# Kernel tuning notes

Measured on AMD Instinct MI355X. Metric: run time of the kernel, lower is better.

## Reference

```python
import jax, jax.numpy as jnp
import numpy as np

EPS = 1e-5

def _layernorm(x, gamma, beta):
    mu = jnp.mean(x, axis=-1, keepdims=True)
    var = jnp.var(x, axis=-1, keepdims=True)
    return (x - mu) * jax.lax.rsqrt(var + EPS) * gamma + beta

def setup_inputs() -> dict:
    key = jax.random.key(0)
    ks = jax.random.split(key, 8)
    B, I, H = 8192, 1024, 1024
    s_w = 1.0 / np.sqrt(I)
    s_u = 1.0 / np.sqrt(H)
    return {
        "x": jax.random.normal(ks[0], (B, I), jnp.float32),
        "h": jax.random.normal(ks[1], (B, H), jnp.float32),
        "c": jax.random.normal(ks[2], (B, H), jnp.float32),
        "W_w": jax.random.uniform(ks[3], (I, 4 * H), jnp.float32, -s_w, s_w),
        "W_b": jax.random.uniform(ks[4], (4 * H,), jnp.float32, -s_w, s_w),
        "U_w": jax.random.uniform(ks[5], (H, 4 * H), jnp.float32, -s_u, s_u),
        "ln_g_gamma": jnp.ones((4 * H,), jnp.float32),
        "ln_g_beta": jnp.zeros((4 * H,), jnp.float32),
        "ln_c_gamma": jnp.ones((H,), jnp.float32),
        "ln_c_beta": jnp.zeros((H,), jnp.float32),
    }

def reference(x, h, c, W_w, W_b, U_w, ln_g_gamma, ln_g_beta, ln_c_gamma, ln_c_beta):
    gates_x = x @ W_w + W_b            # [B, 4H]
    gates_h = h @ U_w                  # [B, 4H]
    gates = gates_x + gates_h + gates_x * gates_h  # multiplicative integration
    gates = _layernorm(gates, ln_g_gamma, ln_g_beta)
    i, f, g, o = jnp.split(gates, 4, axis=-1)
    i = jax.nn.sigmoid(i)
    f = jax.nn.sigmoid(f)
    o = jax.nn.sigmoid(o)
    g = jnp.tanh(g)
    c_new = f * c + i * g
    c_new = _layernorm(c_new, ln_c_gamma, ln_c_beta)
    h_new = o * jnp.tanh(c_new)
    return (h_new, h_new, c_new)
```

## Files before the change

### kernel.cpp

```cpp
#include <hip/hip_runtime.h>
#include <hip/hip_fp16.h>
#include <cstdint>


#define MB (1024ull * 1024ull)

typedef short bf16x8 __attribute__((ext_vector_type(8)));
typedef float f32x4  __attribute__((ext_vector_type(4)));

__device__ __forceinline__ bool bf16_mode(const void* g1) {
    return ((const unsigned short*)g1)[0] == 0x3F80u;
}
__device__ __forceinline__ float b2f(unsigned short u) {
    union { unsigned int i; float f; } v; v.i = ((unsigned int)u) << 16; return v.f;
}
__device__ __forceinline__ unsigned short f2b(float f) {
    unsigned int i = __float_as_uint(f);
    unsigned int r = (i + 0x7FFFu + ((i >> 16) & 1u)) >> 16;
    return (unsigned short)r;
}
__device__ __forceinline__ unsigned short f2h(float f) {
    __half h = __float2half_rn(f);
    return *(unsigned short*)&h;
}
__device__ __forceinline__ void uph8(uint4 v, float* o) {
    unsigned int w[4] = { v.x, v.y, v.z, v.w };
#pragma unroll
    for (int q = 0; q < 4; ++q) {
        __half2 h = *(__half2*)&w[q];
        float2 f = __half22float2(h);
        o[2 * q] = f.x; o[2 * q + 1] = f.y;
    }
}
__device__ __forceinline__ void up4(uint2 v, float* o) {
    o[0] = __uint_as_float(v.x << 16);
    o[1] = __uint_as_float(v.x & 0xFFFF0000u);
    o[2] = __uint_as_float(v.y << 16);
    o[3] = __uint_as_float(v.y & 0xFFFF0000u);
}
__device__ __forceinline__ unsigned int pack2(unsigned short a, unsigned short b) {
    return (unsigned int)a | ((unsigned int)b << 16);
}
__device__ __forceinline__ void ld4(const void* p, size_t idx, bool isbf, float* o) {
    if (isbf) up4(*(const uint2*)((const unsigned short*)p + idx), o);
    else { float4 v = *(const float4*)((const float*)p + idx); o[0]=v.x; o[1]=v.y; o[2]=v.z; o[3]=v.w; }
}
__device__ __forceinline__ float fast_sigmoid(float z) { return 1.f / (1.f + __expf(-z)); }
__device__ __forceinline__ float fast_tanh(float z)    { return 1.f - 2.f / (__expf(2.f * z) + 1.f); }

__device__ __forceinline__ void load_lds16(const unsigned short* g, unsigned short* l) {
    __builtin_amdgcn_global_load_lds(
        (const __attribute__((address_space(1))) unsigned int*)g,
        (__attribute__((address_space(3))) unsigned int*)l,
        16, 0, 0);
}

__global__ __launch_bounds__(256)
void prep_weights(const void* __restrict__ Ww, const void* __restrict__ Uw,
                  const void* __restrict__ g1,
                  unsigned short* __restrict__ Wt, unsigned short* __restrict__ Ut)
{
    const bool isbf = bf16_mode(g1);
    const void* src = blockIdx.z ? Uw : Ww;
    unsigned short* dst = blockIdx.z ? Ut : Wt;
    __shared__ unsigned short tile[64][68];
    const int t  = threadIdx.x;
    const int tx = t & 15;
    const int ty = t >> 4;
    const int bx = blockIdx.x * 64;
    const int by = blockIdx.y * 64;
    if (isbf) {
        const unsigned short* s = (const unsigned short*)src;
#pragma unroll
        for (int it = 0; it < 4; ++it) {
            const int r = ty + it * 16;
            uint2 v = *(const uint2*)(s + (size_t)(by + r) * 4096 + bx + tx * 4);
            tile[r][tx * 4 + 0] = (unsigned short)(v.x & 0xFFFFu);
            tile[r][tx * 4 + 1] = (unsigned short)(v.x >> 16);
            tile[r][tx * 4 + 2] = (unsigned short)(v.y & 0xFFFFu);
            tile[r][tx * 4 + 3] = (unsigned short)(v.y >> 16);
        }
    } else {
        const float* s = (const float*)src;
#pragma unroll
        for (int it = 0; it < 4; ++it) {
            const int r = ty + it * 16;
            float4 v = *(const float4*)(s + (size_t)(by + r) * 4096 + bx + tx * 4);
            tile[r][tx * 4 + 0] = f2b(v.x);
            tile[r][tx * 4 + 1] = f2b(v.y);
            tile[r][tx * 4 + 2] = f2b(v.z);
            tile[r][tx * 4 + 3] = f2b(v.w);
        }
    }
    __syncthreads();
#pragma unroll
    for (int it = 0; it < 4; ++it) {
        const int rn = ty + it * 16;
        const int ck = tx * 4;
        uint2 w;
        w.x = pack2(tile[ck + 0][rn], tile[ck + 1][rn]);
        w.y = pack2(tile[ck + 2][rn], tile[ck + 3][rn]);
        *(uint2*)(dst + (size_t)(bx + rn) * 1024 + by + ck) = w;
    }
}

__global__ __launch_bounds__(256)
void prep_xh(const void* __restrict__ X, const void* __restrict__ Hs,
             const void* __restrict__ g1, void* __restrict__ outb)
{
    if (bf16_mode(g1)) return;
    const float* src = (blockIdx.y == 0) ? (const float*)X : (const float*)Hs;
    unsigned short* dst = (unsigned short*)((char*)outb + (blockIdx.y == 0 ? 48 * MB : 80 * MB));
    const size_t i0 = ((size_t)blockIdx.x * 256 + threadIdx.x) * 8;
    float4 a = *(const float4*)(src + i0);
    float4 b = *(const float4*)(src + i0 + 4);
    uint4 o;
    o.x = pack2(f2b(a.x), f2b(a.y));
    o.y = pack2(f2b(a.z), f2b(a.w));
    o.z = pack2(f2b(b.x), f2b(b.y));
    o.w = pack2(f2b(b.z), f2b(b.w));
    *(uint4*)(dst + i0) = o;
}

__global__ __launch_bounds__(512, 2)
void milstm_gemm(const void* __restrict__ Xraw, const void* __restrict__ Hraw,
                 const void* __restrict__ g1, const void* __restrict__ outb,
                 const unsigned short* __restrict__ Wt,
                 const unsigned short* __restrict__ Ut,
                 unsigned short* __restrict__ Gx, unsigned short* __restrict__ Gh,
                 int m0)
{
    const bool isbf = bf16_mode(g1);
    const int  z    = blockIdx.z;
    const unsigned short* A = z
        ? (isbf ? (const unsigned short*)Hraw : (const unsigned short*)((const char*)outb + 80 * MB))
        : (isbf ? (const unsigned short*)Xraw : (const unsigned short*)((const char*)outb + 48 * MB));
    const unsigned short* Bm = z ? Ut : Wt;
    unsigned short* Gout = z ? Gh : Gx;

    __shared__ __align__(16) unsigned short lds[4][2][8192];

    const int t    = threadIdx.x;
    const int wave = t >> 6;
    const int lane = t & 63;
    const int quad = lane >> 4;
    const int l16  = lane & 15;
    const int wm2  = wave >> 2;
    const int wn4  = wave & 3;

    const int nwg  = gridDim.x * gridDim.y;
    const int wgid = blockIdx.y * gridDim.x + blockIdx.x;
    const int swz  = (wgid & 7) * (nwg >> 3) + (wgid >> 3);
    const int bm   = (swz >> 4) * 256;
    const int bn   = (swz & 15) * 256;

    const int kbsw = (((t & 3) ^ ((t >> 3) & 3)) * 8);
    const unsigned short* sa0 = A  + (size_t)(m0 + bm + (t >> 2)) * 1024 + kbsw;
    const unsigned short* sb0 = Bm + (size_t)(bn + (t >> 2)) * 1024 + kbsw;

#define STAGE(tile, buf) do {                                        \
        const int ko_ = (tile) * 32;                                 \
        load_lds16(sa0 + ko_,          &lds[buf][0][t * 8]);         \
        load_lds16(sa0 + 131072 + ko_, &lds[buf][0][4096 + t * 8]);  \
        load_lds16(sb0 + ko_,          &lds[buf][1][t * 8]);         \
        load_lds16(sb0 + 131072 + ko_, &lds[buf][1][4096 + t * 8]);  \
    } while (0)

    const int kread = (quad ^ ((l16 >> 1) & 3)) * 8;
    const int raoff = (wm2 * 128 + l16) * 32 + kread;
    const int rboff = (wn4 * 64 + l16) * 32 + kread;

#define LDA(DST, BUF) do { _Pragma("unroll")                                  \
        for (int mi = 0; mi < 8; ++mi)                                        \
            DST[mi] = *(const bf16x8*)(&lds[BUF][0][0] + raoff + mi * 512);   \
    } while (0)
#define LDB(DST, BUF) do { _Pragma("unroll")                                  \
        for (int ni = 0; ni < 4; ++ni)                                        \
            DST[ni] = *(const bf16x8*)(&lds[BUF][1][0] + rboff + ni * 512);   \
    } while (0)

#define BAR()  __builtin_amdgcn_s_barrier()
#define VM4()  asm volatile("s_waitcnt vmcnt(4)" ::: "memory")
#define MFMA32(AV, BV) do {                                                   \
        __builtin_amdgcn_s_setprio(1);                                        \
        _Pragma("unroll")                                                     \
        for (int mi = 0; mi < 8; ++mi)                                        \
            _Pragma("unroll")                                                 \
            for (int ni = 0; ni < 4; ++ni)                                    \
                acc[mi][ni] = __builtin_amdgcn_mfma_f32_16x16x32_bf16(        \
                    AV[mi], BV[ni], acc[mi][ni], 0, 0, 0);                    \
        __builtin_amdgcn_s_setprio(0);                                        \
    } while (0)

    f32x4 acc[8][4] = {};
    bf16x8 aP[8], bP[4], aQ[8], bQ[4];

    STAGE(0, 0);
    STAGE(1, 1);
    STAGE(2, 2);
    asm volatile("s_waitcnt vmcnt(8)" ::: "memory");
    BAR();
    LDA(aP, 0); LDB(bP, 0);

    for (int ii = 0; ii < 8; ++ii) {
        const int q = 4 * ii;
        VM4(); BAR();
        STAGE((q + 3) & 31, 3);
        LDA(aQ, 1); LDB(bQ, 1);
        MFMA32(aP, bP);
        VM4(); BAR();
        STAGE((q + 4) & 31, 0);
        LDA(aP, 2); LDB(bP, 2);
        MFMA32(aQ, bQ);
        VM4(); BAR();
        STAGE((q + 5) & 31, 1);
        LDA(aQ, 3); LDB(bQ, 3);
        MFMA32(aP, bP);
        VM4(); BAR();
        STAGE((q + 6) & 31, 2);
        LDA(aP, 0); LDB(bP, 0);
        MFMA32(aQ, bQ);
    }
#undef STAGE
#undef LDA
#undef LDB
#undef BAR
#undef VM4
#undef MFMA32

    const int col0 = bn + wn4 * 64 + l16;
#pragma unroll
    for (int mi = 0; mi < 8; ++mi) {
        const int row0 = bm + wm2 * 128 + mi * 16 + quad * 4;
#pragma unroll
        for (int ni = 0; ni < 4; ++ni) {
            const int col = col0 + ni * 16;
#pragma unroll
            for (int r = 0; r < 4; ++r)
                Gout[(size_t)(row0 + r) * 4096 + col] = f2h(acc[mi][ni][r]);
        }
    }
}

__global__ __launch_bounds__(256)
void milstm_cell(const unsigned short* __restrict__ Gx,
                 const unsigned short* __restrict__ Gh,
                 const void* __restrict__ Wbr,
                 const void* __restrict__ C,
                 const void* __restrict__ g1, const void* __restrict__ b1,
                 const void* __restrict__ g2, const void* __restrict__ b2,
                 void* __restrict__ outb, int m0)
{
    const bool isbf = bf16_mode(g1);
    const int lrow = blockIdx.x;
    const int row  = m0 + lrow;
    const int tid  = threadIdx.x;
    const int lane = tid & 63;
    const int wave = tid >> 6;
    const uint4* gx4 = (const uint4*)(Gx + (size_t)lrow * 4096);
    const uint4* gh4 = (const uint4*)(Gh + (size_t)lrow * 4096);

    __shared__ __align__(16) float srow[4096];
    __shared__ float red[16];

    float s = 0.f, ss = 0.f;
#pragma unroll
    for (int u = 0; u < 2; ++u) {
        const int gbase = (tid * 2 + u) * 8;
        float fx[8], fh[8], bb[8];
        uph8(gx4[tid * 2 + u], fx);
        uph8(gh4[tid * 2 + u], fh);
        ld4(Wbr, gbase, isbf, bb);
        ld4(Wbr, gbase + 4, isbf, bb + 4);
        float g[8];
#pragma unroll
        for (int k = 0; k < 8; ++k) {
            const float ax = fx[k] + bb[k];
            const float v  = ax + fh[k] + ax * fh[k];
            g[k] = v;
            s  += v;
            ss += v * v;
        }
        *(float4*)&srow[gbase]     = make_float4(g[0], g[1], g[2], g[3]);
        *(float4*)&srow[gbase + 4] = make_float4(g[4], g[5], g[6], g[7]);
    }
#pragma unroll
    for (int off = 32; off > 0; off >>= 1) {
        s  += __shfl_xor(s, off, 64);
        ss += __shfl_xor(ss, off, 64);
    }
    if (lane == 0) { red[wave] = s; red[8 + wave] = ss; }
    __syncthreads();
    s  = red[0] + red[1] + red[2] + red[3];
    ss = red[8] + red[9] + red[10] + red[11];
    const float mu   = s * (1.f / 4096.f);
    const float rstd = rsqrtf(fmaxf(ss * (1.f / 4096.f) - mu * mu, 0.f) + 1e-5f);

    const int j0 = tid * 4;
    float xi[4], xf[4], xg[4], cc[4];
    float G1[4], B1[4], ii[4], cn[4], ov[4];

    { float4 v = *(const float4*)&srow[j0];        xi[0]=v.x; xi[1]=v.y; xi[2]=v.z; xi[3]=v.w; }
    { float4 v = *(const float4*)&srow[1024 + j0]; xf[0]=v.x; xf[1]=v.y; xf[2]=v.z; xf[3]=v.w; }
    { float4 v = *(const float4*)&srow[2048 + j0]; xg[0]=v.x; xg[1]=v.y; xg[2]=v.z; xg[3]=v.w; }
    { float4 v = *(const float4*)&srow[3072 + j0]; ov[0]=v.x; ov[1]=v.y; ov[2]=v.z; ov[3]=v.w; }
    ld4(C, (size_t)row * 1024 + j0, isbf, cc);

    ld4(g1, j0, isbf, G1); ld4(b1, j0, isbf, B1);
#pragma unroll
    for (int q = 0; q < 4; ++q) ii[q] = fast_sigmoid((xi[q] - mu) * rstd * G1[q] + B1[q]);
    ld4(g1, 1024 + j0, isbf, G1); ld4(b1, 1024 + j0, isbf, B1);
#pragma unroll
    for (int q = 0; q < 4; ++q) xf[q] = fast_sigmoid((xf[q] - mu) * rstd * G1[q] + B1[q]);
    ld4(g1, 2048 + j0, isbf, G1); ld4(b1, 2048 + j0, isbf, B1);
#pragma unroll
    for (int q = 0; q < 4; ++q) xg[q] = fast_tanh((xg[q] - mu) * rstd * G1[q] + B1[q]);
    ld4(g1, 3072 + j0, isbf, G1); ld4(b1, 3072 + j0, isbf, B1);
#pragma unroll
    for (int q = 0; q < 4; ++q) ov[q] = fast_sigmoid((ov[q] - mu) * rstd * G1[q] + B1[q]);
#pragma unroll
    for (int q = 0; q < 4; ++q) cn[q] = xf[q] * cc[q] + ii[q] * xg[q];

    float s2  = cn[0] + cn[1] + cn[2] + cn[3];
    float ss2 = cn[0]*cn[0] + cn[1]*cn[1] + cn[2]*cn[2] + cn[3]*cn[3];
#pragma unroll
    for (int off = 32; off > 0; off >>= 1) {
        s2  += __shfl_xor(s2, off, 64);
        ss2 += __shfl_xor(ss2, off, 64);
    }
    if (lane == 0) { red[4 + wave] = s2; red[12 + wave] = ss2; }
    __syncthreads();
    s2  = red[4]  + red[5]  + red[6]  + red[7];
    ss2 = red[12] + red[13] + red[14] + red[15];
    const float mu2   = s2 * (1.f / 1024.f);
    const float rstd2 = rsqrtf(fmaxf(ss2 * (1.f / 1024.f) - mu2 * mu2, 0.f) + 1e-5f);

    ld4(g2, j0, isbf, G1);
    ld4(b2, j0, isbf, B1);

    float hv[4], cv[4];
#pragma unroll
    for (int q = 0; q < 4; ++q) {
        cv[q] = (cn[q] - mu2) * rstd2 * G1[q] + B1[q];
        hv[q] = ov[q] * fast_tanh(cv[q]);
    }

    const size_t BH = (size_t)8192 * 1024;
    if (isbf) {
        unsigned short* out = (unsigned short*)outb;
        uint2 hb, cb;
        hb.x = pack2(f2b(hv[0]), f2b(hv[1])); hb.y = pack2(f2b(hv[2]), f2b(hv[3]));
        cb.x = pack2(f2b(cv[0]), f2b(cv[1])); cb.y = pack2(f2b(cv[2]), f2b(cv[3]));
        *(uint2*)(out + (size_t)row * 1024 + j0)          = hb;
        *(uint2*)(out + BH + (size_t)row * 1024 + j0)     = hb;
        *(uint2*)(out + 2 * BH + (size_t)row * 1024 + j0) = cb;
    } else {
        float* out = (float*)outb;
        float4 hf = { hv[0], hv[1], hv[2], hv[3] };
        float4 cf = { cv[0], cv[1], cv[2], cv[3] };
        *(float4*)(out + (size_t)row * 1024 + j0)          = hf;
        *(float4*)(out + BH + (size_t)row * 1024 + j0)     = hf;
        *(float4*)(out + 2 * BH + (size_t)row * 1024 + j0) = cf;
    }
}

extern "C" void kernel_launch(void* const* d_in, const int* in_sizes, int n_in,
                              void* d_out, int out_size, void* d_ws, size_t ws_size,
                              hipStream_t stream)
{
    const void* X  = d_in[0];
    const void* Hh = d_in[1];
    const void* C  = d_in[2];
    const void* Ww = d_in[3];
    const void* Wb = d_in[4];
    const void* Uw = d_in[5];
    const void* g1 = d_in[6];
    const void* b1 = d_in[7];
    const void* g2 = d_in[8];
    const void* b2 = d_in[9];

    const int P  = (ws_size >= 144 * MB) ? 1 : ((ws_size >= 80 * MB) ? 2 : 4);
    const int MR = 8192 / P;
    const size_t gsz = (size_t)MR * 4096;
    unsigned short* Gx = (unsigned short*)d_ws;
    unsigned short* Gh = Gx + gsz;
    unsigned short* Wt = Gh + gsz;
    unsigned short* Ut = Wt + (size_t)4096 * 1024;

    prep_weights<<<dim3(64, 16, 2), 256, 0, stream>>>(Ww, Uw, g1, Wt, Ut);
    prep_xh<<<dim3(4096, 2), 256, 0, stream>>>(X, Hh, g1, d_out);

    for (int ph = 0; ph < P; ++ph) {
        const int m0 = ph * MR;
        milstm_gemm<<<dim3(16, MR / 256, 2), 512, 0, stream>>>(
            X, Hh, g1, d_out, Wt, Ut, Gx, Gh, m0);
        milstm_cell<<<dim3(MR), 256, 0, stream>>>(
            Gx, Gh, Wb, C, g1, b1, g2, b2, d_out, m0);
    }
}
```

Before: 417.7 us.

## Merge prep kernels, fold bias into GEMM epilogue, use one wave per row in cell

The two preprocessing kernels become one launch that dispatches on block index, removing a launch. The x-side bias is added in the GEMM epilogue before the fp16 store, so the cell kernel no longer loads W_b. The cell kernel now gives each row to a single wave that keeps all 4096 gate values in registers. This drops the LDS staging buffer and both block-level syncs, in exchange for higher register pressure per thread. Adding the bias before rounding to fp16 also changes numerics slightly.

```diff
diff --git a/kernel.cpp b/kernel.cpp
--- a/kernel.cpp
+++ b/kernel.cpp
@@ -32,18 +32,20 @@
         o[2 * q] = f.x; o[2 * q + 1] = f.y;
     }
 }
-__device__ __forceinline__ void up4(uint2 v, float* o) {
-    o[0] = __uint_as_float(v.x << 16);
-    o[1] = __uint_as_float(v.x & 0xFFFF0000u);
-    o[2] = __uint_as_float(v.y << 16);
-    o[3] = __uint_as_float(v.y & 0xFFFF0000u);
-}
 __device__ __forceinline__ unsigned int pack2(unsigned short a, unsigned short b) {
     return (unsigned int)a | ((unsigned int)b << 16);
 }
 __device__ __forceinline__ void ld4(const void* p, size_t idx, bool isbf, float* o) {
-    if (isbf) up4(*(const uint2*)((const unsigned short*)p + idx), o);
-    else { float4 v = *(const float4*)((const float*)p + idx); o[0]=v.x; o[1]=v.y; o[2]=v.z; o[3]=v.w; }
+    if (isbf) {
+        uint2 v = *(const uint2*)((const unsigned short*)p + idx);
+        o[0] = __uint_as_float(v.x << 16);
+        o[1] = __uint_as_float(v.x & 0xFFFF0000u);
+        o[2] = __uint_as_float(v.y << 16);
+        o[3] = __uint_as_float(v.y & 0xFFFF0000u);
+    } else {
+        float4 v = *(const float4*)((const float*)p + idx);
+        o[0]=v.x; o[1]=v.y; o[2]=v.z; o[3]=v.w;
+    }
 }
 __device__ __forceinline__ float fast_sigmoid(float z) { return 1.f / (1.f + __expf(-z)); }
 __device__ __forceinline__ float fast_tanh(float z)    { return 1.f - 2.f / (__expf(2.f * z) + 1.f); }
@@ -56,75 +58,82 @@
 }
 
 __global__ __launch_bounds__(256)
-void prep_weights(const void* __restrict__ Ww, const void* __restrict__ Uw,
-                  const void* __restrict__ g1,
-                  unsigned short* __restrict__ Wt, unsigned short* __restrict__ Ut)
+void milstm_prep(const void* __restrict__ Ww, const void* __restrict__ Uw,
+                 const void* __restrict__ X, const void* __restrict__ Hs,
+                 const void* __restrict__ g1,
+                 unsigned short* __restrict__ Wt, unsigned short* __restrict__ Ut,
+                 void* __restrict__ outb)
 {
     const bool isbf = bf16_mode(g1);
-    const void* src = blockIdx.z ? Uw : Ww;
-    unsigned short* dst = blockIdx.z ? Ut : Wt;
+    const int bid = blockIdx.x;
+    const int t   = threadIdx.x;
     __shared__ unsigned short tile[64][68];
-    const int t  = threadIdx.x;
-    const int tx = t & 15;
-    const int ty = t >> 4;
-    const int bx = blockIdx.x * 64;
-    const int by = blockIdx.y * 64;
-    if (isbf) {
-        const unsigned short* s = (const unsigned short*)src;
+
+    if (bid < 2048) {
+        const int wz  = bid >> 10;
+        const int idx = bid & 1023;
+        const int bx  = (idx & 63) * 64;
+        const int by  = (idx >> 6) * 64;
+        const void* src = wz ? Uw : Ww;
+        unsigned short* dst = wz ? Ut : Wt;
+        const int tx = t & 15;
+        const int ty = t >> 4;
+        if (isbf) {
+            const unsigned short* s = (const unsigned short*)src;
+#pragma unroll
+            for (int it = 0; it < 4; ++it) {
+                const int r = ty + it * 16;
+                uint2 v = *(const uint2*)(s + (size_t)(by + r) * 4096 + bx + tx * 4);
+                tile[r][tx * 4 + 0] = (unsigned short)(v.x & 0xFFFFu);
+                tile[r][tx * 4 + 1] = (unsigned short)(v.x >> 16);
+                tile[r][tx * 4 + 2] = (unsigned short)(v.y & 0xFFFFu);
+                tile[r][tx * 4 + 3] = (unsigned short)(v.y >> 16);
+            }
+        } else {
+            const float* s = (const float*)src;
+#pragma unroll
+            for (int it = 0; it < 4; ++it) {
+                const int r = ty + it * 16;
+                float4 v = *(const float4*)(s + (size_t)(by + r) * 4096 + bx + tx * 4);
+                tile[r][tx * 4 + 0] = f2b(v.x);
+                tile[r][tx * 4 + 1] = f2b(v.y);
+                tile[r][tx * 4 + 2] = f2b(v.z);
+                tile[r][tx * 4 + 3] = f2b(v.w);
+            }
+        }
+        __syncthreads();
 #pragma unroll
         for (int it = 0; it < 4; ++it) {
-            const int r = ty + it * 16;
-            uint2 v = *(const uint2*)(s + (size_t)(by + r) * 4096 + bx + tx * 4);
-            tile[r][tx * 4 + 0] = (unsigned short)(v.x & 0xFFFFu);
-            tile[r][tx * 4 + 1] = (unsigned short)(v.x >> 16);
-            tile[r][tx * 4 + 2] = (unsigned short)(v.y & 0xFFFFu);
-            tile[r][tx * 4 + 3] = (unsigned short)(v.y >> 16);
+            const int rn = ty + it * 16;
+            const int ck = tx * 4;
+            uint2 w;
+            w.x = pack2(tile[ck + 0][rn], tile[ck + 1][rn]);
+            w.y = pack2(tile[ck + 2][rn], tile[ck + 3][rn]);
+            *(uint2*)(dst + (size_t)(bx + rn) * 1024 + by + ck) = w;
         }
     } else {
-        const float* s = (const float*)src;
-#pragma unroll
-        for (int it = 0; it < 4; ++it) {
-            const int r = ty + it * 16;
-            float4 v = *(const float4*)(s + (size_t)(by + r) * 4096 + bx + tx * 4);
-            tile[r][tx * 4 + 0] = f2b(v.x);
-            tile[r][tx * 4 + 1] = f2b(v.y);
-            tile[r][tx * 4 + 2] = f2b(v.z);
-            tile[r][tx * 4 + 3] = f2b(v.w);
-        }
-    }
-    __syncthreads();
-#pragma unroll
-    for (int it = 0; it < 4; ++it) {
-        const int rn = ty + it * 16;
-        const int ck = tx * 4;
-        uint2 w;
-        w.x = pack2(tile[ck + 0][rn], tile[ck + 1][rn]);
-        w.y = pack2(tile[ck + 2][rn], tile[ck + 3][rn]);
-        *(uint2*)(dst + (size_t)(bx + rn) * 1024 + by + ck) = w;
-    }
-}
-
-__global__ __launch_bounds__(256)
-void prep_xh(const void* __restrict__ X, const void* __restrict__ Hs,
-             const void* __restrict__ g1, void* __restrict__ outb)
-{
-    if (bf16_mode(g1)) return;
-    const float* src = (blockIdx.y == 0) ? (const float*)X : (const float*)Hs;
-    unsigned short* dst = (unsigned short*)((char*)outb + (blockIdx.y == 0 ? 48 * MB : 80 * MB));
-    const size_t i0 = ((size_t)blockIdx.x * 256 + threadIdx.x) * 8;
-    float4 a = *(const float4*)(src + i0);
-    float4 b = *(const float4*)(src + i0 + 4);
-    uint4 o;
-    o.x = pack2(f2b(a.x), f2b(a.y));
-    o.y = pack2(f2b(a.z), f2b(a.w));
-    o.z = pack2(f2b(b.x), f2b(b.y));
-    o.w = pack2(f2b(b.z), f2b(b.w));
-    *(uint4*)(dst + i0) = o;
+        if (isbf) return;
+        const int idx = bid - 2048;
+        const int yy  = idx >> 12;
+        const int sub = idx & 4095;
+        const float* src = yy ? (const float*)Hs : (const float*)X;
+        unsigned short* dst = (unsigned short*)((char*)outb + (yy ? 80 * MB : 48 * MB));
+        const size_t i0 = ((size_t)sub * 256 + t) * 8;
+        float4 a = *(const float4*)(src + i0);
+        float4 b = *(const float4*)(src + i0 + 4);
+        uint4 o;
+        o.x = pack2(f2b(a.x), f2b(a.y));
+        o.y = pack2(f2b(a.z), f2b(a.w));
+        o.z = pack2(f2b(b.x), f2b(b.y));
+        o.w = pack2(f2b(b.z), f2b(b.w));
+        *(uint4*)(dst + i0) = o;
+    }
 }
 
 __global__ __launch_bounds__(512, 2)
 void milstm_gemm(const void* __restrict__ Xraw, const void* __restrict__ Hraw,
-                 const void* __restrict__ g1, const void* __restrict__ outb,
+                 const void* __restrict__ g1, const void* __restrict__ Wbr,
+                 const void* __restrict__ outb,
                  const unsigned short* __restrict__ Wt,
                  const unsigned short* __restrict__ Ut,
                  unsigned short* __restrict__ Gx, unsigned short* __restrict__ Gh,
@@ -229,6 +238,13 @@
 #undef MFMA32
 
     const int col0 = bn + wn4 * 64 + l16;
+    float bias_[4] = {0.f, 0.f, 0.f, 0.f};
+    if (z == 0) {
+#pragma unroll
+        for (int ni = 0; ni < 4; ++ni)
+            bias_[ni] = isbf ? b2f(((const unsigned short*)Wbr)[col0 + ni * 16])
+                             : ((const float*)Wbr)[col0 + ni * 16];
+    }
 #pragma unroll
     for (int mi = 0; mi < 8; ++mi) {
         const int row0 = bm + wm2 * 128 + mi * 16 + quad * 4;
@@ -237,7 +253,7 @@
             const int col = col0 + ni * 16;
 #pragma unroll
             for (int r = 0; r < 4; ++r)
-                Gout[(size_t)(row0 + r) * 4096 + col] = f2h(acc[mi][ni][r]);
+                Gout[(size_t)(row0 + r) * 4096 + col] = f2h(acc[mi][ni][r] + bias_[ni]);
         }
     }
 }
@@ -245,122 +261,120 @@
 __global__ __launch_bounds__(256)
 void milstm_cell(const unsigned short* __restrict__ Gx,
                  const unsigned short* __restrict__ Gh,
-                 const void* __restrict__ Wbr,
                  const void* __restrict__ C,
                  const void* __restrict__ g1, const void* __restrict__ b1,
                  const void* __restrict__ g2, const void* __restrict__ b2,
                  void* __restrict__ outb, int m0)
 {
     const bool isbf = bf16_mode(g1);
-    const int lrow = blockIdx.x;
+    const int lane = threadIdx.x & 63;
+    const int lrow = blockIdx.x * 4 + (threadIdx.x >> 6);
     const int row  = m0 + lrow;
-    const int tid  = threadIdx.x;
-    const int lane = tid & 63;
-    const int wave = tid >> 6;
-    const uint4* gx4 = (const uint4*)(Gx + (size_t)lrow * 4096);
-    const uint4* gh4 = (const uint4*)(Gh + (size_t)lrow * 4096);
-
-    __shared__ __align__(16) float srow[4096];
-    __shared__ float red[16];
-
+
+    const uint4* gx4 = (const uint4*)Gx + (size_t)lrow * 512 + lane;
+    const uint4* gh4 = (const uint4*)Gh + (size_t)lrow * 512 + lane;
+
+    float v[8][8];
     float s = 0.f, ss = 0.f;
 #pragma unroll
-    for (int u = 0; u < 2; ++u) {
-        const int gbase = (tid * 2 + u) * 8;
-        float fx[8], fh[8], bb[8];
-        uph8(gx4[tid * 2 + u], fx);
-        uph8(gh4[tid * 2 + u], fh);
-        ld4(Wbr, gbase, isbf, bb);
-        ld4(Wbr, gbase + 4, isbf, bb + 4);
-        float g[8];
-#pragma unroll
-        for (int k = 0; k < 8; ++k) {
-            const float ax = fx[k] + bb[k];
-            const float v  = ax + fh[k] + ax * fh[k];
-            g[k] = v;
-            s  += v;
-            ss += v * v;
-        }
-        *(float4*)&srow[gbase]     = make_float4(g[0], g[1], g[2], g[3]);
-        *(float4*)&srow[gbase + 4] = make_float4(g[4], g[5], g[6], g[7]);
+    for (int k = 0; k < 8; ++k) {
+        float fx[8], fh[8];
+        uph8(gx4[k * 64], fx);
+        uph8(gh4[k * 64], fh);
+#pragma unroll
+        for (int e = 0; e < 8; ++e) {
+            const float val = fx[e] + fh[e] + fx[e] * fh[e];
+            v[k][e] = val;
+            s  += val;
+            ss += val * val;
+        }
     }
 #pragma unroll
     for (int off = 32; off > 0; off >>= 1) {
         s  += __shfl_xor(s, off, 64);
         ss += __shfl_xor(ss, off, 64);
     }
-    if (lane == 0) { red[wave] = s; red[8 + wave] = ss; }
-    __syncthreads();
-    s  = red[0] + red[1] + red[2] + red[3];
-    ss = red[8] + red[9] + red[10] + red[11];
     const float mu   = s * (1.f / 4096.f);
     const float rstd = rsqrtf(fmaxf(ss * (1.f / 4096.f) - mu * mu, 0.f) + 1e-5f);
 
-    const int j0 = tid * 4;
-    float xi[4], xf[4], xg[4], cc[4];
-    float G1[4], B1[4], ii[4], cn[4], ov[4];
-
-    { float4 v = *(const float4*)&srow[j0];        xi[0]=v.x; xi[1]=v.y; xi[2]=v.z; xi[3]=v.w; }
-    { float4 v = *(const float4*)&srow[1024 + j0]; xf[0]=v.x; xf[1]=v.y; xf[2]=v.z; xf[3]=v.w; }
-    { float4 v = *(const float4*)&srow[2048 + j0]; xg[0]=v.x; xg[1]=v.y; xg[2]=v.z; xg[3]=v.w; }
-    { float4 v = *(const float4*)&srow[3072 + j0]; ov[0]=v.x; ov[1]=v.y; ov[2]=v.z; ov[3]=v.w; }
-    ld4(C, (size_t)row * 1024 + j0, isbf, cc);
-
-    ld4(g1, j0, isbf, G1); ld4(b1, j0, isbf, B1);
-#pragma unroll
-    for (int q = 0; q < 4; ++q) ii[q] = fast_sigmoid((xi[q] - mu) * rstd * G1[q] + B1[q]);
-    ld4(g1, 1024 + j0, isbf, G1); ld4(b1, 1024 + j0, isbf, B1);
-#pragma unroll
-    for (int q = 0; q < 4; ++q) xf[q] = fast_sigmoid((xf[q] - mu) * rstd * G1[q] + B1[q]);
-    ld4(g1, 2048 + j0, isbf, G1); ld4(b1, 2048 + j0, isbf, B1);
-#pragma unroll
-    for (int q = 0; q < 4; ++q) xg[q] = fast_tanh((xg[q] - mu) * rstd * G1[q] + B1[q]);
-    ld4(g1, 3072 + j0, isbf, G1); ld4(b1, 3072 + j0, isbf, B1);
-#pragma unroll
-    for (int q = 0; q < 4; ++q) ov[q] = fast_sigmoid((ov[q] - mu) * rstd * G1[q] + B1[q]);
-#pragma unroll
-    for (int q = 0; q < 4; ++q) cn[q] = xf[q] * cc[q] + ii[q] * xg[q];
-
-    float s2  = cn[0] + cn[1] + cn[2] + cn[3];
-    float ss2 = cn[0]*cn[0] + cn[1]*cn[1] + cn[2]*cn[2] + cn[3]*cn[3];
+    float cn[2][8], ov[2][8];
+    float s2 = 0.f, ss2 = 0.f;
+#pragma unroll
+    for (int jc = 0; jc < 2; ++jc) {
+        const int base = jc * 512 + lane * 8;
+        float G1[8], B1[8], t8[8], cc[8];
+        ld4(g1, base, isbf, G1);     ld4(g1, base + 4, isbf, G1 + 4);
+        ld4(b1, base, isbf, B1);     ld4(b1, base + 4, isbf, B1 + 4);
+        float ii[8];
+#pragma unroll
+        for (int e = 0; e < 8; ++e) ii[e] = fast_sigmoid((v[jc][e] - mu) * rstd * G1[e] + B1[e]);
+        ld4(g1, 1024 + base, isbf, G1); ld4(g1, 1024 + base + 4, isbf, G1 + 4);
+        ld4(b1, 1024 + base, isbf, B1); ld4(b1, 1024 + base + 4, isbf, B1 + 4);
+#pragma unroll
+        for (int e = 0; e < 8; ++e) t8[e] = fast_sigmoid((v[2 + jc][e] - mu) * rstd * G1[e] + B1[e]);
+        ld4(g1, 2048 + base, isbf, G1); ld4(g1, 2048 + base + 4, isbf, G1 + 4);
+        ld4(b1, 2048 + base, isbf, B1); ld4(b1, 2048 + base + 4, isbf, B1 + 4);
+        float gg[8];
+#pragma unroll
+        for (int e = 0; e < 8; ++e) gg[e] = fast_tanh((v[4 + jc][e] - mu) * rstd * G1[e] + B1[e]);
+        ld4(g1, 3072 + base, isbf, G1); ld4(g1, 3072 + base + 4, isbf, G1 + 4);
+        ld4(b1, 3072 + base, isbf, B1); ld4(b1, 3072 + base + 4, isbf, B1 + 4);
+#pragma unroll
+        for (int e = 0; e < 8; ++e) ov[jc][e] = fast_sigmoid((v[6 + jc][e] - mu) * rstd * G1[e] + B1[e]);
+        ld4(C, (size_t)row * 1024 + base, isbf, cc);
+        ld4(C, (size_t)row * 1024 + base + 4, isbf, cc + 4);
+#pragma unroll
+        for (int e = 0; e < 8; ++e) {
+            const float c2 = t8[e] * cc[e] + ii[e] * gg[e];
+            cn[jc][e] = c2;
+            s2  += c2;
+            ss2 += c2 * c2;
+        }
+    }
 #pragma unroll
     for (int off = 32; off > 0; off >>= 1) {
         s2  += __shfl_xor(s2, off, 64);
         ss2 += __shfl_xor(ss2, off, 64);
     }
-    if (lane == 0) { red[4 + wave] = s2; red[12 + wave] = ss2; }
-    __syncthreads();
-    s2  = red[4]  + red[5]  + red[6]  + red[7];
-    ss2 = red[12] + red[13] + red[14] + red[15];
     const float mu2   = s2 * (1.f / 1024.f);
     const float rstd2 = rsqrtf(fmaxf(ss2 * (1.f / 1024.f) - mu2 * mu2, 0.f) + 1e-5f);
 
-    ld4(g2, j0, isbf, G1);
-    ld4(b2, j0, isbf, B1);
-
-    float hv[4], cv[4];
-#pragma unroll
-    for (int q = 0; q < 4; ++q) {
-        cv[q] = (cn[q] - mu2) * rstd2 * G1[q] + B1[q];
-        hv[q] = ov[q] * fast_tanh(cv[q]);
-    }
-
     const size_t BH = (size_t)8192 * 1024;
-    if (isbf) {
-        unsigned short* out = (unsigned short*)outb;
-        uint2 hb, cb;
-        hb.x = pack2(f2b(hv[0]), f2b(hv[1])); hb.y = pack2(f2b(hv[2]), f2b(hv[3]));
-        cb.x = pack2(f2b(cv[0]), f2b(cv[1])); cb.y = pack2(f2b(cv[2]), f2b(cv[3]));
-        *(uint2*)(out + (size_t)row * 1024 + j0)          = hb;
-        *(uint2*)(out + BH + (size_t)row * 1024 + j0)     = hb;
-        *(uint2*)(out + 2 * BH + (size_t)row * 1024 + j0) = cb;
-    } else {
-        float* out = (float*)outb;
-        float4 hf = { hv[0], hv[1], hv[2], hv[3] };
-        float4 cf = { cv[0], cv[1], cv[2], cv[3] };
-        *(float4*)(out + (size_t)row * 1024 + j0)          = hf;
-        *(float4*)(out + BH + (size_t)row * 1024 + j0)     = hf;
-        *(float4*)(out + 2 * BH + (size_t)row * 1024 + j0) = cf;
+#pragma unroll
+    for (int jc = 0; jc < 2; ++jc) {
+        const int base = jc * 512 + lane * 8;
+        float G2[8], B2[8], hv[8], cv[8];
+        ld4(g2, base, isbf, G2); ld4(g2, base + 4, isbf, G2 + 4);
+        ld4(b2, base, isbf, B2); ld4(b2, base + 4, isbf, B2 + 4);
+#pragma unroll
+        for (int e = 0; e < 8; ++e) {
+            cv[e] = (cn[jc][e] - mu2) * rstd2 * G2[e] + B2[e];
+            hv[e] = ov[jc][e] * fast_tanh(cv[e]);
+        }
+        const size_t o0 = (size_t)row * 1024 + base;
+        if (isbf) {
+            unsigned short* out = (unsigned short*)outb;
+            uint4 hb, cb;
+            hb.x = pack2(f2b(hv[0]), f2b(hv[1])); hb.y = pack2(f2b(hv[2]), f2b(hv[3]));
+            hb.z = pack2(f2b(hv[4]), f2b(hv[5])); hb.w = pack2(f2b(hv[6]), f2b(hv[7]));
+            cb.x = pack2(f2b(cv[0]), f2b(cv[1])); cb.y = pack2(f2b(cv[2]), f2b(cv[3]));
+            cb.z = pack2(f2b(cv[4]), f2b(cv[5])); cb.w = pack2(f2b(cv[6]), f2b(cv[7]));
+            *(uint4*)(out + o0)          = hb;
+            *(uint4*)(out + BH + o0)     = hb;
+            *(uint4*)(out + 2 * BH + o0) = cb;
+        } else {
+            float* out = (float*)outb;
+            float4 h0 = { hv[0], hv[1], hv[2], hv[3] };
+            float4 h1 = { hv[4], hv[5], hv[6], hv[7] };
+            float4 c0 = { cv[0], cv[1], cv[2], cv[3] };
+            float4 c1 = { cv[4], cv[5], cv[6], cv[7] };
+            *(float4*)(out + o0)              = h0;
+            *(float4*)(out + o0 + 4)          = h1;
+            *(float4*)(out + BH + o0)         = h0;
+            *(float4*)(out + BH + o0 + 4)     = h1;
+            *(float4*)(out + 2 * BH + o0)     = c0;
+            *(float4*)(out + 2 * BH + o0 + 4) = c1;
+        }
     }
 }
 
@@ -387,14 +401,13 @@
     unsigned short* Wt = Gh + gsz;
     unsigned short* Ut = Wt + (size_t)4096 * 1024;
 
-    prep_weights<<<dim3(64, 16, 2), 256, 0, stream>>>(Ww, Uw, g1, Wt, Ut);
-    prep_xh<<<dim3(4096, 2), 256, 0, stream>>>(X, Hh, g1, d_out);
+    milstm_prep<<<dim3(10240), 256, 0, stream>>>(Ww, Uw, X, Hh, g1, Wt, Ut, d_out);
 
     for (int ph = 0; ph < P; ++ph) {
         const int m0 = ph * MR;
         milstm_gemm<<<dim3(16, MR / 256, 2), 512, 0, stream>>>(
-            X, Hh, g1, d_out, Wt, Ut, Gx, Gh, m0);
-        milstm_cell<<<dim3(MR), 256, 0, stream>>>(
-            Gx, Gh, Wb, C, g1, b1, g2, b2, d_out, m0);
-    }
-}
+            X, Hh, g1, Wb, d_out, Wt, Ut, Gx, Gh, m0);
+        milstm_cell<<<dim3(MR / 4), 256, 0, stream>>>(
+            Gx, Gh, C, g1, b1, g2, b2, d_out, m0);
+    }
+}
```

Measured after the change: 408.7 us. -2.2%, faster.
